# Kernel optimization log

Hardware: AMD Instinct MI355X
Metric: run time of the kernel (lower is better)

The kernel has to match this reference:

```python
import jax, jax.numpy as jnp
import numpy as np

B, N, H, T = 2048, 512, 20, 3

def setup_inputs() -> dict:
    key = jax.random.key(0)
    ks = jax.random.split(key, 10)
    x = jax.random.normal(ks[0], (B, N, H), dtype=jnp.float32)
    # row-stochastic-ish adjacency so time-step iteration stays numerically tame
    A_in = jax.random.uniform(ks[1], (N, N), dtype=jnp.float32) / N
    std = 0.05
    W3w = jax.random.normal(ks[2], (H, 2 * H), dtype=jnp.float32) * std
    W3u = jax.random.normal(ks[3], (H, H), dtype=jnp.float32) * std
    W4w = jax.random.normal(ks[4], (H, 2 * H), dtype=jnp.float32) * std
    W4u = jax.random.normal(ks[5], (H, H), dtype=jnp.float32) * std
    W5w = jax.random.normal(ks[6], (H, 2 * H), dtype=jnp.float32) * std
    W5u = jax.random.normal(ks[7], (H, H), dtype=jnp.float32) * std
    W_out = jax.random.normal(ks[8], (H, 2 * H), dtype=jnp.float32) * std
    b_out = jnp.zeros((H,), dtype=jnp.float32)
    return {"x": x, "A_in": A_in, "W3w": W3w, "W3u": W3u, "W4w": W4w,
            "W4u": W4u, "W5w": W5w, "W5u": W5u, "W_out": W_out, "b_out": b_out}

def reference(x, A_in, W3w, W3u, W4w, W4u, W5w, W5u, W_out, b_out):
    # x: [B, N, H]; A_in: [N, N]; out-matrix is the transpose of in-matrix.
    A_out = A_in.T
    b, n, h = x.shape
    x_flat = x.reshape(b * n, h)              # original 'input' kept for skip-cat
    nodes = x                                  # batch_aog_nodes [B, N, H]
    outputs = []
    for _ in range(T):
        # aggregation: in- and out-neighborhood bmm, then concat -> [B*N, 2H]
        agg_in = jnp.einsum('nm,bmh->bnh', A_in, nodes)
        agg_out = jnp.einsum('nm,bmh->bnh', A_out, nodes)
        av = jnp.concatenate([agg_in, agg_out], axis=-1).reshape(b * n, 2 * h)
        fn = nodes.reshape(b * n, h)
        # GRU-style gates
        zv = jax.nn.sigmoid(av @ W3w.T + fn @ W3u.T)
        rv = jax.nn.sigmoid(av @ W4w.T + fn @ W4u.T)
        hv = jnp.tanh(av @ W5w.T + (rv * fn) @ W5u.T)
        fn = (1.0 - zv) * fn + zv * hv
        nodes = fn.reshape(b, n, h)
        step = jnp.concatenate([fn, x_flat], axis=1) @ W_out.T + b_out
        outputs.append(step.reshape(b, n, -1))
    return jnp.stack(outputs, axis=0)  # [T, B, N, out]; torch returns this as a list per step
```

## Files before the change

### kernel.cpp

```cpp
#include <hip/hip_runtime.h>
#include <stdint.h>

#define B_SZ 2048
#define N_SZ 512
#define H_SZ 20
#define T_STEPS 3

typedef unsigned short u16;
typedef __attribute__((ext_vector_type(8))) short bf8;
typedef __attribute__((ext_vector_type(4))) float f4;

#define MFMA(a, b, c) __builtin_amdgcn_mfma_f32_16x16x32_bf16((a), (b), (c), 0, 0, 0)

__device__ __forceinline__ u16 f2bf(float f) {
    union { float f; uint32_t u; } v; v.f = f;
    uint32_t u = v.u;
    u += 0x7FFFu + ((u >> 16) & 1u);
    return (u16)(u >> 16);
}
__device__ __forceinline__ float bf2f(u16 h) {
    union { uint32_t u; float f; } v; v.u = ((uint32_t)h) << 16;
    return v.f;
}
__device__ __forceinline__ int scoff(int c, int f) {
    return c * 64 + (((f >> 3) ^ (c & 7)) << 3) + (f & 7);
}
__device__ __forceinline__ float sigm(float x) { return 1.f / (1.f + __expf(-x)); }


__global__ void prep_nodes(const float* __restrict__ x, u16* __restrict__ nodes) {
    __shared__ float xt[N_SZ * H_SZ];
    int b = blockIdx.x;
    const float* xb = x + (size_t)b * N_SZ * H_SZ;
    for (int i = threadIdx.x; i < N_SZ * H_SZ; i += 256) xt[i] = xb[i];
    __syncthreads();
    u16* nb = nodes + (size_t)b * (N_SZ * H_SZ);
    for (int i = threadIdx.x; i < N_SZ * H_SZ; i += 256) {
        int nt = i / 320;
        int r  = i - nt * 320;
        int hp = r >> 4, nl = r & 15;
        int n = nt * 16 + nl;
        nb[i] = f2bf(xt[n * H_SZ + hp]);
    }
}

__global__ void prep_xo(const float* __restrict__ x, const float* __restrict__ Wout,
                        const float* __restrict__ bout, u16* __restrict__ xo) {
    int i = blockIdx.x * 256 + threadIdx.x;
    const float* xv = x + (size_t)i * H_SZ;
    float xl[H_SZ];
    #pragma unroll
    for (int h = 0; h < H_SZ; h++) xl[h] = xv[h];
    u16* o = xo + (size_t)i * H_SZ;
    for (int hp = 0; hp < H_SZ; hp++) {
        float s = bout[hp];
        const float* wr = Wout + hp * 2 * H_SZ + H_SZ;
        #pragma unroll
        for (int h = 0; h < H_SZ; h++) s += xl[h] * wr[h];
        o[hp] = f2bf(s);
    }
}

__global__ void prep_afrag(const float* __restrict__ A, u16* __restrict__ pAT,
                           u16* __restrict__ pA) {
    int idx = blockIdx.x * 256 + threadIdx.x;
    int lane = idx & 63;
    int kt = (idx >> 6) & 15;
    int nt = idx >> 10;
    int n = nt * 16 + (lane & 15);
    int k0 = kt * 32 + (lane >> 4) * 8;
    u16* d1 = pAT + (size_t)idx * 8;
    u16* d2 = pA + (size_t)idx * 8;
    #pragma unroll
    for (int j = 0; j < 8; j++) {
        int m = k0 + j;
        d1[j] = f2bf(A[(size_t)n * N_SZ + m]);
        d2[j] = f2bf(A[(size_t)m * N_SZ + n]);
    }
}

__global__ void prep_wfrag(const float* __restrict__ W3w, const float* __restrict__ W3u,
                           const float* __restrict__ W4w, const float* __restrict__ W4u,
                           const float* __restrict__ W5w, const float* __restrict__ W5u,
                           const float* __restrict__ Wout,
                           u16* __restrict__ wbig, u16* __restrict__ whu, u16* __restrict__ wo1) {
    int t = blockIdx.x * 256 + threadIdx.x;
    int lane = t & 63;
    int l16 = lane & 15, quad = lane >> 4;
    if (t < 768) {
        int kt = (t >> 6) & 1;
        int mt = t >> 7;
        int mrow = mt * 16 + l16;
        int g = mrow >> 5, lr = mrow & 31;
        u16* d = wbig + (size_t)t * 8;
        #pragma unroll
        for (int j = 0; j < 8; j++) {
            int k = kt * 32 + quad * 8 + j;
            float v = 0.f;
            if (lr < 20) {
                if (k < 40) {
                    const float* W = (g == 0) ? W3w : (g == 1) ? W4w : W5w;
                    v = W[lr * 40 + k];
                } else if (k < 60 && g < 2) {
                    const float* U = (g == 0) ? W3u : W4u;
                    v = U[lr * 20 + (k - 40)];
                }
            }
            d[j] = f2bf(v);
        }
    } else if (t < 896) {
        int tt = t - 768;
        int mrow = (tt >> 6) * 16 + l16;
        u16* d = whu + (size_t)tt * 8;
        #pragma unroll
        for (int j = 0; j < 8; j++) {
            int k = quad * 8 + j;
            d[j] = f2bf((mrow < 20 && k < 20) ? W5u[mrow * 20 + k] : 0.f);
        }
    } else {
        int tt = t - 896;
        int mrow = (tt >> 6) * 16 + l16;
        u16* d = wo1 + (size_t)tt * 8;
        #pragma unroll
        for (int j = 0; j < 8; j++) {
            int k = quad * 8 + j;
            d[j] = f2bf((mrow < 20 && k < 20) ? Wout[mrow * 40 + k] : 0.f);
        }
    }
}

__global__ void ws_too_small(float* out) { out[0] = 12345.0f; }

__global__ __launch_bounds__(256, 2)
void step_kernel(const u16* __restrict__ pAT, const u16* __restrict__ pA,
                 const u16* __restrict__ wbig, const u16* __restrict__ whu,
                 const u16* __restrict__ wo1, const u16* __restrict__ xo,
                 u16* __restrict__ nodes, float* __restrict__ out)
{
    __shared__ __align__(16) u16 lds_all[40 * 512 + 4 * 2048];
    u16* Xs = lds_all;
    int tid = threadIdx.x;
    int wv = tid >> 6, lane = tid & 63;
    int l16 = lane & 15, quad = lane >> 4;
    int b0 = blockIdx.x * 2;
    u16* scw = lds_all + 40 * 512 + wv * 2048;

    const u16* nb = nodes + (size_t)b0 * (N_SZ * H_SZ);

    #pragma unroll 1
    for (int t = 0; t < T_STEPS; t++) {
        #pragma unroll
        for (int i = 0; i < 10; i++) {
            int idx = i * 256 + tid;
            uint4 v = *(const uint4*)(nb + (size_t)idx * 8);
            int bs = idx >= 1280 ? 1 : 0;
            int idxb = idx - bs * 1280;
            int nt = idxb / 40;
            int r  = idxb - nt * 40;
            int hp = r >> 1;
            int half = r & 1;
            int row = bs * 20 + hp;
            int mb = nt * 2 + half;
            *(uint4*)&Xs[row * 512 + ((mb ^ (row & 7)) << 3)] = v;
        }
        __syncthreads();

        for (int p = 0; p < 4; p++) {
            int nt0 = wv * 8 + p * 2;

            f4 acc[2][3][2];
            #pragma unroll
            for (int a0 = 0; a0 < 2; a0++)
                #pragma unroll
                for (int a1 = 0; a1 < 3; a1++)
                    #pragma unroll
                    for (int a2 = 0; a2 < 2; a2++)
                        acc[a0][a1][a2] = (f4){0.f, 0.f, 0.f, 0.f};

            for (int kt = 0; kt < 16; kt++) {
                bf8 af[3];
                #pragma unroll
                for (int mt = 0; mt < 3; mt++) {
                    int row = mt * 16 + l16;
                    int kb = (kt * 4 + quad) ^ (row & 7);
                    af[mt] = *(const bf8*)&Xs[row * 512 + kb * 8];
                }
                #pragma unroll
                for (int ntL = 0; ntL < 2; ntL++) {
                    size_t fo = ((size_t)((nt0 + ntL) * 16 + kt) * 64 + lane) * 8;
                    bf8 bi = *(const bf8*)(pAT + fo);
                    bf8 bo = *(const bf8*)(pA + fo);
                    #pragma unroll
                    for (int mt = 0; mt < 3; mt++) {
                        acc[ntL][mt][0] = MFMA(af[mt], bi, acc[ntL][mt][0]);
                        acc[ntL][mt][1] = MFMA(af[mt], bo, acc[ntL][mt][1]);
                    }
                }
            }

            #pragma unroll
            for (int ntL = 0; ntL < 2; ntL++) {
                int nt = nt0 + ntL;
                int nglob = nt * 16 + l16;

                #pragma unroll
                for (int mt = 0; mt < 3; mt++) {
                    if (mt < 2 || quad < 2) {
                        int row0 = mt * 16 + quad * 4;
                        int bs = (row0 >= 20) ? 1 : 0;
                        int h0 = row0 - bs * 20;
                        int c = bs * 16 + l16;
                        #pragma unroll
                        for (int r = 0; r < 4; r++) {
                            scw[scoff(c, h0 + r)]      = f2bf(acc[ntL][mt][0][r]);
                            scw[scoff(c, 20 + h0 + r)] = f2bf(acc[ntL][mt][1][r]);
                        }
                    }
                }
                {
                    int c = lane & 31;
                    int h0 = (lane >> 5) * 10;
                    int bs = c >> 4, nl = c & 15;
                    int m = nt * 16 + nl;
                    int mb = m >> 3, mo = m & 7;
                    #pragma unroll
                    for (int i = 0; i < 10; i++) {
                        int h = h0 + i;
                        int row = bs * 20 + h;
                        u16 v = Xs[row * 512 + ((mb ^ (row & 7)) << 3) + mo];
                        scw[scoff(c, 40 + h)] = v;
                    }
                    if (lane < 32) {
                        #pragma unroll
                        for (int f = 60; f < 64; f++) scw[scoff(c, f)] = 0;
                    }
                }

                f4 g1[6][2];
                #pragma unroll
                for (int a0 = 0; a0 < 6; a0++) { g1[a0][0] = (f4){0,0,0,0}; g1[a0][1] = (f4){0,0,0,0}; }
                #pragma unroll
                for (int kt = 0; kt < 2; kt++) {
                    bf8 bfr[2];
                    #pragma unroll
                    for (int ct = 0; ct < 2; ct++) {
                        int c = ct * 16 + l16;
                        int fb = (kt * 4 + quad) ^ (c & 7);
                        bfr[ct] = *(const bf8*)&scw[c * 64 + fb * 8];
                    }
                    #pragma unroll
                    for (int mt = 0; mt < 6; mt++) {
                        bf8 wf = *(const bf8*)(wbig + ((size_t)(mt * 2 + kt) * 64 + lane) * 8);
                        g1[mt][0] = MFMA(wf, bfr[0], g1[mt][0]);
                        g1[mt][1] = MFMA(wf, bfr[1], g1[mt][1]);
                    }
                }

                #pragma unroll
                for (int ct = 0; ct < 2; ct++) {
                    int c = ct * 16 + l16;
                    #pragma unroll
                    for (int r = 0; r < 4; r++) {
                        int hp = quad * 4 + r;
                        float fn = bf2f(scw[scoff(c, 40 + hp)]);
                        scw[scoff(c, hp)] = f2bf(sigm(g1[2][ct][r]) * fn);
                    }
                    if (quad == 0) {
                        #pragma unroll
                        for (int r = 0; r < 4; r++) {
                            int hp = 16 + r;
                            float fn = bf2f(scw[scoff(c, 40 + hp)]);
                            scw[scoff(c, hp)] = f2bf(sigm(g1[3][ct][r]) * fn);
                        }
                    }
                }

                f4 hu[2][2];
                hu[0][0] = (f4){0,0,0,0}; hu[0][1] = (f4){0,0,0,0};
                hu[1][0] = (f4){0,0,0,0}; hu[1][1] = (f4){0,0,0,0};
                #pragma unroll
                for (int ct = 0; ct < 2; ct++) {
                    int c = ct * 16 + l16;
                    int fb = quad ^ (c & 7);
                    bf8 bfr = *(const bf8*)&scw[c * 64 + fb * 8];
                    #pragma unroll
                    for (int mt = 0; mt < 2; mt++) {
                        bf8 wf = *(const bf8*)(whu + ((size_t)(mt * 64) + lane) * 8);
                        hu[mt][ct] = MFMA(wf, bfr, hu[mt][ct]);
                    }
                }

                #pragma unroll
                for (int ct = 0; ct < 2; ct++) {
                    int c = ct * 16 + l16;
                    size_t nbase = ((size_t)(b0 + ct) * 32 + nt) * 320 + l16;
                    #pragma unroll
                    for (int r = 0; r < 4; r++) {
                        int hp = quad * 4 + r;
                        float fn = bf2f(scw[scoff(c, 40 + hp)]);
                        float z = sigm(g1[0][ct][r]);
                        float hpre = g1[4][ct][r] + hu[0][ct][r];
                        float hv = 2.f / (1.f + __expf(-2.f * hpre)) - 1.f;
                        u16 w = f2bf((1.f - z) * fn + z * hv);
                        nodes[nbase + (size_t)hp * 16] = w;
                        scw[scoff(c, hp)] = w;
                    }
                    if (quad == 0) {
                        #pragma unroll
                        for (int r = 0; r < 4; r++) {
                            int hp = 16 + r;
                            float fn = bf2f(scw[scoff(c, 40 + hp)]);
                            float z = sigm(g1[1][ct][r]);
                            float hpre = g1[5][ct][r] + hu[1][ct][r];
                            float hv = 2.f / (1.f + __expf(-2.f * hpre)) - 1.f;
                            u16 w = f2bf((1.f - z) * fn + z * hv);
                            nodes[nbase + (size_t)hp * 16] = w;
                            scw[scoff(c, hp)] = w;
                        }
                    }
                }

                f4 og[2][2];
                og[0][0] = (f4){0,0,0,0}; og[0][1] = (f4){0,0,0,0};
                og[1][0] = (f4){0,0,0,0}; og[1][1] = (f4){0,0,0,0};
                #pragma unroll
                for (int ct = 0; ct < 2; ct++) {
                    int c = ct * 16 + l16;
                    int fb = quad ^ (c & 7);
                    bf8 bfr = *(const bf8*)&scw[c * 64 + fb * 8];
                    #pragma unroll
                    for (int mt = 0; mt < 2; mt++) {
                        bf8 wf = *(const bf8*)(wo1 + ((size_t)(mt * 64) + lane) * 8);
                        og[mt][ct] = MFMA(wf, bfr, og[mt][ct]);
                    }
                }

                #pragma unroll
                for (int ct = 0; ct < 2; ct++) {
                    int bg = b0 + ct;
                    size_t xob = ((size_t)bg * N_SZ + nglob) * H_SZ;
                    size_t ob = (((size_t)t * B_SZ + bg) * N_SZ + nglob) * H_SZ;
                    {
                        f4 v;
                        #pragma unroll
                        for (int r = 0; r < 4; r++) v[r] = og[0][ct][r] + bf2f(xo[xob + quad * 4 + r]);
                        *(f4*)(out + ob + quad * 4) = v;
                    }
                    if (quad == 0) {
                        f4 v;
                        #pragma unroll
                        for (int r = 0; r < 4; r++) v[r] = og[1][ct][r] + bf2f(xo[xob + 16 + r]);
                        *(f4*)(out + ob + 16) = v;
                    }
                }
            }
        }
        if (t < T_STEPS - 1) __syncthreads();
    }
}

#define WS_NODES   0
#define WS_XO      41943040UL
#define WS_PAT     83886080UL
#define WS_PA      84410368UL
#define WS_WBIG    84934656UL
#define WS_WHU     84946944UL
#define WS_WO1     84948992UL
#define WS_NEEDED  84951040UL

extern "C" void kernel_launch(void* const* d_in, const int* in_sizes, int n_in,
                              void* d_out, int out_size, void* d_ws, size_t ws_size,
                              hipStream_t stream) {
    const float* x    = (const float*)d_in[0];
    const float* A    = (const float*)d_in[1];
    const float* W3w  = (const float*)d_in[2];
    const float* W3u  = (const float*)d_in[3];
    const float* W4w  = (const float*)d_in[4];
    const float* W4u  = (const float*)d_in[5];
    const float* W5w  = (const float*)d_in[6];
    const float* W5u  = (const float*)d_in[7];
    const float* Wout = (const float*)d_in[8];
    const float* bout = (const float*)d_in[9];
    float* out = (float*)d_out;

    if (ws_size < WS_NEEDED) {
        ws_too_small<<<1, 1, 0, stream>>>(out);
        return;
    }
    char* ws = (char*)d_ws;
    u16* nodes = (u16*)(ws + WS_NODES);
    u16* xo    = (u16*)(ws + WS_XO);
    u16* pAT   = (u16*)(ws + WS_PAT);
    u16* pA    = (u16*)(ws + WS_PA);
    u16* wbig  = (u16*)(ws + WS_WBIG);
    u16* whu   = (u16*)(ws + WS_WHU);
    u16* wo1   = (u16*)(ws + WS_WO1);

    prep_nodes<<<B_SZ, 256, 0, stream>>>(x, nodes);
    prep_xo<<<(B_SZ * N_SZ) / 256, 256, 0, stream>>>(x, Wout, bout, xo);
    prep_afrag<<<128, 256, 0, stream>>>(A, pAT, pA);
    prep_wfrag<<<4, 256, 0, stream>>>(W3w, W3u, W4w, W4u, W5w, W5u, Wout, wbig, whu, wo1);

    step_kernel<<<B_SZ / 2, 256, 0, stream>>>(pAT, pA, wbig, whu, wo1, xo, nodes, out);
}
```

Before: 831.7 us.

## Fuse node and skip-projection prep kernels and vectorize LDS/global bf16 accesses

Merges prep_nodes and prep_xo into one kernel, so x is read from global memory once and staged in shared memory for both the transposed bf16 node layout and the x·W_out skip projection. Stores there are widened to 8-element and 4-element vectors. In the step kernel, scalar bf16 LDS stores and loads are replaced with packed uint2/uint32 accesses, and fn values are kept in registers instead of being re-read. The hardware __bf16 conversion replaces the manual rounding code. The goal is fewer memory transactions and instructions; the trade-off is higher register pressure and shared memory per block in the prep kernel.

```diff
diff --git a/kernel.cpp b/kernel.cpp
--- a/kernel.cpp
+++ b/kernel.cpp
@@ -13,51 +13,76 @@
 #define MFMA(a, b, c) __builtin_amdgcn_mfma_f32_16x16x32_bf16((a), (b), (c), 0, 0, 0)
 
 __device__ __forceinline__ u16 f2bf(float f) {
-    union { float f; uint32_t u; } v; v.f = f;
-    uint32_t u = v.u;
-    u += 0x7FFFu + ((u >> 16) & 1u);
-    return (u16)(u >> 16);
+    __bf16 h = (__bf16)f;
+    union { __bf16 b; u16 u; } v; v.b = h;
+    return v.u;
 }
 __device__ __forceinline__ float bf2f(u16 h) {
     union { uint32_t u; float f; } v; v.u = ((uint32_t)h) << 16;
     return v.f;
 }
+__device__ __forceinline__ uint32_t pk2(float a, float b) {
+    return (uint32_t)f2bf(a) | ((uint32_t)f2bf(b) << 16);
+}
+__device__ __forceinline__ uint2 pack4(f4 v) {
+    uint2 r; r.x = pk2(v[0], v[1]); r.y = pk2(v[2], v[3]); return r;
+}
 __device__ __forceinline__ int scoff(int c, int f) {
     return c * 64 + (((f >> 3) ^ (c & 7)) << 3) + (f & 7);
 }
 __device__ __forceinline__ float sigm(float x) { return 1.f / (1.f + __expf(-x)); }
 
 
-__global__ void prep_nodes(const float* __restrict__ x, u16* __restrict__ nodes) {
+__global__ __launch_bounds__(256)
+void prep_fused(const float* __restrict__ x, const float* __restrict__ Wout,
+                const float* __restrict__ bout,
+                u16* __restrict__ nodes, u16* __restrict__ xo) {
     __shared__ float xt[N_SZ * H_SZ];
+    __shared__ float wo2[H_SZ * H_SZ];
+    __shared__ float bo[H_SZ];
+    int tid = threadIdx.x;
     int b = blockIdx.x;
-    const float* xb = x + (size_t)b * N_SZ * H_SZ;
-    for (int i = threadIdx.x; i < N_SZ * H_SZ; i += 256) xt[i] = xb[i];
+    const float4* xb4 = (const float4*)(x + (size_t)b * (N_SZ * H_SZ));
+    #pragma unroll
+    for (int i = 0; i < 10; i++) ((float4*)xt)[i * 256 + tid] = xb4[i * 256 + tid];
+    for (int i = tid; i < H_SZ * H_SZ; i += 256)
+        wo2[i] = Wout[(i / H_SZ) * 2 * H_SZ + H_SZ + (i % H_SZ)];
+    if (tid < H_SZ) bo[tid] = bout[tid];
     __syncthreads();
+
     u16* nb = nodes + (size_t)b * (N_SZ * H_SZ);
-    for (int i = threadIdx.x; i < N_SZ * H_SZ; i += 256) {
-        int nt = i / 320;
-        int r  = i - nt * 320;
-        int hp = r >> 4, nl = r & 15;
-        int n = nt * 16 + nl;
-        nb[i] = f2bf(xt[n * H_SZ + hp]);
-    }
-}
-
-__global__ void prep_xo(const float* __restrict__ x, const float* __restrict__ Wout,
-                        const float* __restrict__ bout, u16* __restrict__ xo) {
-    int i = blockIdx.x * 256 + threadIdx.x;
-    const float* xv = x + (size_t)i * H_SZ;
-    float xl[H_SZ];
     #pragma unroll
-    for (int h = 0; h < H_SZ; h++) xl[h] = xv[h];
-    u16* o = xo + (size_t)i * H_SZ;
-    for (int hp = 0; hp < H_SZ; hp++) {
-        float s = bout[hp];
-        const float* wr = Wout + hp * 2 * H_SZ + H_SZ;
-        #pragma unroll
-        for (int h = 0; h < H_SZ; h++) s += xl[h] * wr[h];
-        o[hp] = f2bf(s);
+    for (int g0 = 0; g0 < 5; g0++) {
+        int g = g0 * 256 + tid;
+        int nt = g / 40, r = g - nt * 40;
+        int hp = r >> 1, nl0 = (r & 1) * 8;
+        union { uint4 v; u16 s[8]; } u;
+        #pragma unroll
+        for (int j = 0; j < 8; j++) u.s[j] = f2bf(xt[(nt * 16 + nl0 + j) * H_SZ + hp]);
+        *(uint4*)&nb[(size_t)g * 8] = u.v;
+    }
+
+    u16* ob = xo + (size_t)b * (N_SZ * H_SZ);
+    #pragma unroll
+    for (int n0 = 0; n0 < 2; n0++) {
+        int n = n0 * 256 + tid;
+        float xl[H_SZ];
+        #pragma unroll
+        for (int h = 0; h < H_SZ; h++) xl[h] = xt[n * H_SZ + h];
+        #pragma unroll
+        for (int q = 0; q < 5; q++) {
+            float s[4];
+            #pragma unroll
+            for (int k = 0; k < 4; k++) {
+                int hp = q * 4 + k;
+                float acc = bo[hp];
+                #pragma unroll
+                for (int h = 0; h < H_SZ; h++) acc += xl[h] * wo2[hp * H_SZ + h];
+                s[k] = acc;
+            }
+            uint2 v; v.x = pk2(s[0], s[1]); v.y = pk2(s[2], s[3]);
+            *(uint2*)&ob[(size_t)n * H_SZ + q * 4] = v;
+        }
     }
 }
 
@@ -210,11 +235,8 @@
                         int bs = (row0 >= 20) ? 1 : 0;
                         int h0 = row0 - bs * 20;
                         int c = bs * 16 + l16;
-                        #pragma unroll
-                        for (int r = 0; r < 4; r++) {
-                            scw[scoff(c, h0 + r)]      = f2bf(acc[ntL][mt][0][r]);
-                            scw[scoff(c, 20 + h0 + r)] = f2bf(acc[ntL][mt][1][r]);
-                        }
+                        *(uint2*)&scw[scoff(c, h0)]      = pack4(acc[ntL][mt][0]);
+                        *(uint2*)&scw[scoff(c, 20 + h0)] = pack4(acc[ntL][mt][1]);
                     }
                 }
                 {
@@ -223,16 +245,26 @@
                     int bs = c >> 4, nl = c & 15;
                     int m = nt * 16 + nl;
                     int mb = m >> 3, mo = m & 7;
+                    u16 fnv[10];
                     #pragma unroll
                     for (int i = 0; i < 10; i++) {
-                        int h = h0 + i;
-                        int row = bs * 20 + h;
-                        u16 v = Xs[row * 512 + ((mb ^ (row & 7)) << 3) + mo];
-                        scw[scoff(c, 40 + h)] = v;
-                    }
-                    if (lane < 32) {
-                        #pragma unroll
-                        for (int f = 60; f < 64; f++) scw[scoff(c, f)] = 0;
+                        int row = bs * 20 + h0 + i;
+                        fnv[i] = Xs[row * 512 + ((mb ^ (row & 7)) << 3) + mo];
+                    }
+                    if (h0 == 0) {
+                        uint2 a; a.x = fnv[0] | (fnv[1] << 16); a.y = fnv[2] | (fnv[3] << 16);
+                        *(uint2*)&scw[scoff(c, 40)] = a;
+                        uint2 b2; b2.x = fnv[4] | (fnv[5] << 16); b2.y = fnv[6] | (fnv[7] << 16);
+                        *(uint2*)&scw[scoff(c, 44)] = b2;
+                        *(uint32_t*)&scw[scoff(c, 48)] = (uint32_t)fnv[8] | ((uint32_t)fnv[9] << 16);
+                    } else {
+                        *(uint32_t*)&scw[scoff(c, 50)] = (uint32_t)fnv[0] | ((uint32_t)fnv[1] << 16);
+                        uint2 a; a.x = fnv[2] | (fnv[3] << 16); a.y = fnv[4] | (fnv[5] << 16);
+                        *(uint2*)&scw[scoff(c, 52)] = a;
+                        uint2 b2; b2.x = fnv[6] | (fnv[7] << 16); b2.y = fnv[8] | (fnv[9] << 16);
+                        *(uint2*)&scw[scoff(c, 56)] = b2;
+                        uint2 z; z.x = 0u; z.y = 0u;
+                        *(uint2*)&scw[scoff(c, 60)] = z;
                     }
                 }
 
@@ -256,22 +288,25 @@
                     }
                 }
 
+                float fnr[2][4], fnr2[2][4];
                 #pragma unroll
                 for (int ct = 0; ct < 2; ct++) {
                     int c = ct * 16 + l16;
-                    #pragma unroll
-                    for (int r = 0; r < 4; r++) {
-                        int hp = quad * 4 + r;
-                        float fn = bf2f(scw[scoff(c, 40 + hp)]);
-                        scw[scoff(c, hp)] = f2bf(sigm(g1[2][ct][r]) * fn);
-                    }
+                    uint2 fl = *(const uint2*)&scw[scoff(c, 40 + quad * 4)];
+                    fnr[ct][0] = bf2f((u16)fl.x);  fnr[ct][1] = bf2f((u16)(fl.x >> 16));
+                    fnr[ct][2] = bf2f((u16)fl.y);  fnr[ct][3] = bf2f((u16)(fl.y >> 16));
+                    uint2 rp;
+                    rp.x = pk2(sigm(g1[2][ct][0]) * fnr[ct][0], sigm(g1[2][ct][1]) * fnr[ct][1]);
+                    rp.y = pk2(sigm(g1[2][ct][2]) * fnr[ct][2], sigm(g1[2][ct][3]) * fnr[ct][3]);
+                    *(uint2*)&scw[scoff(c, quad * 4)] = rp;
                     if (quad == 0) {
-                        #pragma unroll
-                        for (int r = 0; r < 4; r++) {
-                            int hp = 16 + r;
-                            float fn = bf2f(scw[scoff(c, 40 + hp)]);
-                            scw[scoff(c, hp)] = f2bf(sigm(g1[3][ct][r]) * fn);
-                        }
+                        uint2 fl2 = *(const uint2*)&scw[scoff(c, 56)];
+                        fnr2[ct][0] = bf2f((u16)fl2.x);  fnr2[ct][1] = bf2f((u16)(fl2.x >> 16));
+                        fnr2[ct][2] = bf2f((u16)fl2.y);  fnr2[ct][3] = bf2f((u16)(fl2.y >> 16));
+                        uint2 rp2;
+                        rp2.x = pk2(sigm(g1[3][ct][0]) * fnr2[ct][0], sigm(g1[3][ct][1]) * fnr2[ct][1]);
+                        rp2.y = pk2(sigm(g1[3][ct][2]) * fnr2[ct][2], sigm(g1[3][ct][3]) * fnr2[ct][3]);
+                        *(uint2*)&scw[scoff(c, 16)] = rp2;
                     }
                 }
 
@@ -294,29 +329,35 @@
                 for (int ct = 0; ct < 2; ct++) {
                     int c = ct * 16 + l16;
                     size_t nbase = ((size_t)(b0 + ct) * 32 + nt) * 320 + l16;
+                    float w4[4];
                     #pragma unroll
                     for (int r = 0; r < 4; r++) {
-                        int hp = quad * 4 + r;
-                        float fn = bf2f(scw[scoff(c, 40 + hp)]);
                         float z = sigm(g1[0][ct][r]);
                         float hpre = g1[4][ct][r] + hu[0][ct][r];
                         float hv = 2.f / (1.f + __expf(-2.f * hpre)) - 1.f;
-                        u16 w = f2bf((1.f - z) * fn + z * hv);
-                        nodes[nbase + (size_t)hp * 16] = w;
-                        scw[scoff(c, hp)] = w;
-                    }
+                        w4[r] = (1.f - z) * fnr[ct][r] + z * hv;
+                    }
+                    uint2 wp; wp.x = pk2(w4[0], w4[1]); wp.y = pk2(w4[2], w4[3]);
+                    *(uint2*)&scw[scoff(c, quad * 4)] = wp;
+                    nodes[nbase + (size_t)(quad * 4 + 0) * 16] = (u16)wp.x;
+                    nodes[nbase + (size_t)(quad * 4 + 1) * 16] = (u16)(wp.x >> 16);
+                    nodes[nbase + (size_t)(quad * 4 + 2) * 16] = (u16)wp.y;
+                    nodes[nbase + (size_t)(quad * 4 + 3) * 16] = (u16)(wp.y >> 16);
                     if (quad == 0) {
+                        float w42[4];
                         #pragma unroll
                         for (int r = 0; r < 4; r++) {
-                            int hp = 16 + r;
-                            float fn = bf2f(scw[scoff(c, 40 + hp)]);
                             float z = sigm(g1[1][ct][r]);
                             float hpre = g1[5][ct][r] + hu[1][ct][r];
                             float hv = 2.f / (1.f + __expf(-2.f * hpre)) - 1.f;
-                            u16 w = f2bf((1.f - z) * fn + z * hv);
-                            nodes[nbase + (size_t)hp * 16] = w;
-                            scw[scoff(c, hp)] = w;
+                            w42[r] = (1.f - z) * fnr2[ct][r] + z * hv;
                         }
+                        uint2 wp2; wp2.x = pk2(w42[0], w42[1]); wp2.y = pk2(w42[2], w42[3]);
+                        *(uint2*)&scw[scoff(c, 16)] = wp2;
+                        nodes[nbase + (size_t)16 * 16] = (u16)wp2.x;
+                        nodes[nbase + (size_t)17 * 16] = (u16)(wp2.x >> 16);
+                        nodes[nbase + (size_t)18 * 16] = (u16)wp2.y;
+                        nodes[nbase + (size_t)19 * 16] = (u16)(wp2.y >> 16);
                     }
                 }
 
@@ -341,15 +382,21 @@
                     size_t xob = ((size_t)bg * N_SZ + nglob) * H_SZ;
                     size_t ob = (((size_t)t * B_SZ + bg) * N_SZ + nglob) * H_SZ;
                     {
+                        uint2 xp = *(const uint2*)(xo + xob + quad * 4);
                         f4 v;
-                        #pragma unroll
-                        for (int r = 0; r < 4; r++) v[r] = og[0][ct][r] + bf2f(xo[xob + quad * 4 + r]);
+                        v[0] = og[0][ct][0] + bf2f((u16)xp.x);
+                        v[1] = og[0][ct][1] + bf2f((u16)(xp.x >> 16));
+                        v[2] = og[0][ct][2] + bf2f((u16)xp.y);
+                        v[3] = og[0][ct][3] + bf2f((u16)(xp.y >> 16));
                         *(f4*)(out + ob + quad * 4) = v;
                     }
                     if (quad == 0) {
+                        uint2 xp = *(const uint2*)(xo + xob + 16);
                         f4 v;
-                        #pragma unroll
-                        for (int r = 0; r < 4; r++) v[r] = og[1][ct][r] + bf2f(xo[xob + 16 + r]);
+                        v[0] = og[1][ct][0] + bf2f((u16)xp.x);
+                        v[1] = og[1][ct][1] + bf2f((u16)(xp.x >> 16));
+                        v[2] = og[1][ct][2] + bf2f((u16)xp.y);
+                        v[3] = og[1][ct][3] + bf2f((u16)(xp.y >> 16));
                         *(f4*)(out + ob + 16) = v;
                     }
                 }
@@ -396,8 +443,7 @@
     u16* whu   = (u16*)(ws + WS_WHU);
     u16* wo1   = (u16*)(ws + WS_WO1);
 
-    prep_nodes<<<B_SZ, 256, 0, stream>>>(x, nodes);
-    prep_xo<<<(B_SZ * N_SZ) / 256, 256, 0, stream>>>(x, Wout, bout, xo);
+    prep_fused<<<B_SZ, 256, 0, stream>>>(x, Wout, bout, nodes, xo);
     prep_afrag<<<128, 256, 0, stream>>>(A, pAT, pA);
     prep_wfrag<<<4, 256, 0, stream>>>(W3w, W3u, W4w, W4u, W5w, W5u, Wout, wbig, whu, wo1);
 
```

After: 774.1 us. 1.07x faster.
